# Kernel optimization log

Hardware: AMD Instinct MI355X
Metric: run time of the kernel (lower is better)

Reference implementation:

```python
import jax, jax.numpy as jnp
import numpy as np


def setup_inputs() -> dict:
    key = jax.random.key(0)
    ks = jax.random.split(key, 6)
    B, T, E = 4, 1024, 1024
    H, D = 16, 64  # num_heads = embed_size // head_size
    s = 0.02
    x = jax.random.normal(ks[0], (B, T, E), dtype=jnp.float32)
    Wq = jax.random.normal(ks[1], (H, D, E), dtype=jnp.float32) * s
    Wk = jax.random.normal(ks[2], (H, D, E), dtype=jnp.float32) * s
    Wv = jax.random.normal(ks[3], (H, D, E), dtype=jnp.float32) * s
    Wp = jax.random.normal(ks[4], (E, E), dtype=jnp.float32) * s
    bp = jnp.zeros((E,), dtype=jnp.float32)
    return {"x": x, "Wq": Wq, "Wk": Wk, "Wv": Wv, "Wp": Wp, "bp": bp}


def reference(x, Wq, Wk, Wv, Wp, bp):
    # x: [B, T, E]; Wq/Wk/Wv: [H, D, E] (per-head Linear(E, D, bias=False) weights)
    B, T, E = x.shape
    H, D, _ = Wq.shape
    scale = 1.0 / jnp.sqrt(jnp.asarray(D, dtype=x.dtype))
    # per-head projections, vectorized over heads (same math as the ModuleList loop)
    q = jnp.einsum('bte,hde->bhtd', x, Wq)
    k = jnp.einsum('bte,hde->bhtd', x, Wk)
    v = jnp.einsum('bte,hde->bhtd', x, Wv)
    scores = jnp.einsum('bhtd,bhsd->bhts', q, k) * scale  # [B,H,T,T]
    causal = jnp.tril(jnp.ones((T, T), dtype=bool))
    scores = jnp.where(causal[None, None], scores, jnp.finfo(x.dtype).min)
    att = jax.nn.softmax(scores, axis=-1)  # attention dropout: identity in eval
    o = jnp.einsum('bhts,bhsd->bhtd', att, v)
    # concat heads along channel dim (head order = module list order)
    o = o.transpose(0, 2, 1, 3).reshape(B, T, H * D)
    # output projection (nn.Linear: y = o @ Wp.T + bp); dropout: identity in eval
    return o @ Wp.T + bp
```

## Files before the change

kernel.cpp:

```cpp
#include <hip/hip_runtime.h>


#define T_SZ 1024
#define E_SZ 1024
#define H_SZ 16
#define D_SZ 64

typedef __attribute__((ext_vector_type(8))) short bf16x8;
typedef __attribute__((ext_vector_type(4))) short bf16x4;
typedef __attribute__((ext_vector_type(4))) float f32x4;

static __device__ __forceinline__ unsigned short f2b(float f) {
  unsigned int u = __builtin_bit_cast(unsigned int, f);
  u += 0x7fffu + ((u >> 16) & 1u);
  return (unsigned short)(u >> 16);
}

static __device__ __forceinline__ unsigned int cvt_pk(float lo, float hi) {
  unsigned int r;
  asm("v_cvt_pk_bf16_f32 %0, %1, %2" : "=v"(r) : "v"(lo), "v"(hi));
  return r;
}

static __device__ __forceinline__ void load_lds16(const void* g, void* l) {
  __builtin_amdgcn_global_load_lds(
      (const __attribute__((address_space(1))) void*)g,
      (__attribute__((address_space(3))) void*)l, 16, 0, 0);
}

__global__ void cast_all(const float* __restrict__ x, const float* __restrict__ wq,
                         const float* __restrict__ wk, const float* __restrict__ wv,
                         const float* __restrict__ wp,
                         unsigned short* __restrict__ xb,
                         unsigned short* __restrict__ wqkvb,
                         unsigned short* __restrict__ wpb) {
  int b = blockIdx.x;
  const float4* src;
  ushort4* dst;
  int i;
  if (b < 4096) {
    src = (const float4*)x; dst = (ushort4*)xb; i = b * 256 + threadIdx.x;
  } else {
    int a = (b - 4096) >> 10;
    i = ((b - 4096) & 1023) * 256 + threadIdx.x;
    src = (const float4*)(a == 0 ? wq : a == 1 ? wk : a == 2 ? wv : wp);
    dst = (ushort4*)(a == 3 ? wpb : wqkvb + (size_t)a * 1048576);
  }
  float4 v = src[i];
  ushort4 o;
  o.x = f2b(v.x); o.y = f2b(v.y); o.z = f2b(v.z); o.w = f2b(v.w);
  dst[i] = o;
}

template <int EPI, int BN>
__global__ void gemm_bt(const unsigned short* __restrict__ A,
                        const unsigned short* __restrict__ Bm,
                        int M, int N, int K,
                        float* __restrict__ outF, const float* __restrict__ bias,
                        unsigned short* __restrict__ Qb,
                        unsigned short* __restrict__ Kb,
                        unsigned short* __restrict__ Vtb) {
  constexpr int ASZ = 16384;
  constexpr int BSZ = BN * 128;
  constexpr int SLOT = ASZ + BSZ;
  constexpr int NN = BN / 32;
  __shared__ __align__(16) char lds[2 * SLOT];
  const int tid = threadIdx.x;
  const int wid = tid >> 6;
  const int lane = tid & 63;
  const int llo = lane & 15, lhi = lane >> 4;
  const int row0 = blockIdx.x * 128, col0 = blockIdx.y * BN;
  const int wr = (wid >> 1) * 64, wc = (wid & 1) * (BN / 2);
  const int swl = ((llo >> 2) & 3) << 5;

  f32x4 acc[4][NN];
#pragma unroll
  for (int m = 0; m < 4; ++m)
#pragma unroll
    for (int n = 0; n < NN; ++n) {
      f32x4 z = {0.f, 0.f, 0.f, 0.f};
      acc[m][n] = z;
    }

  auto stage = [&](int kt, char* base) {
#pragma unroll
    for (int c = 0; c < 4; ++c) {
      int off = c * 4096 + tid * 16;
      int r = off >> 7, cb = off & 127;
      int sb = cb ^ (((r >> 2) & 3) << 5);
      load_lds16((const char*)A + ((size_t)(row0 + r) * K + kt) * 2 + sb,
                 base + c * 4096 + wid * 1024);
    }
#pragma unroll
    for (int c = 0; c < BSZ / 4096; ++c) {
      int off = c * 4096 + tid * 16;
      int r = off >> 7, cb = off & 127;
      int sb = cb ^ (((r >> 2) & 3) << 5);
      load_lds16((const char*)Bm + ((size_t)(col0 + r) * K + kt) * 2 + sb,
                 base + ASZ + c * 4096 + wid * 1024);
    }
  };

  stage(0, lds);
  __syncthreads();
  int buf = 0;

  for (int kt = 0; kt < K; kt += 64) {
    char* cur = lds + buf * SLOT;
    if (kt + 64 < K) stage(kt + 64, lds + (buf ^ 1) * SLOT);

    bf16x8 af[4][2], bfr[NN][2];
#pragma unroll
    for (int m = 0; m < 4; ++m)
#pragma unroll
      for (int kk = 0; kk < 2; ++kk)
        af[m][kk] = *reinterpret_cast<const bf16x8*>(
            cur + (wr + m * 16 + llo) * 128 + ((kk * 64 + lhi * 16) ^ swl));
#pragma unroll
    for (int n = 0; n < NN; ++n)
#pragma unroll
      for (int kk = 0; kk < 2; ++kk)
        bfr[n][kk] = *reinterpret_cast<const bf16x8*>(
            cur + ASZ + (wc + n * 16 + llo) * 128 + ((kk * 64 + lhi * 16) ^ swl));
#pragma unroll
    for (int m = 0; m < 4; ++m)
#pragma unroll
      for (int n = 0; n < NN; ++n)
#pragma unroll
        for (int kk = 0; kk < 2; ++kk)
          acc[m][n] = __builtin_amdgcn_mfma_f32_16x16x32_bf16(af[m][kk], bfr[n][kk],
                                                              acc[m][n], 0, 0, 0);
    __syncthreads();
    buf ^= 1;
  }

#pragma unroll
  for (int m = 0; m < 4; ++m)
#pragma unroll
    for (int n = 0; n < NN; ++n) {
      const int grow0 = row0 + wr + m * 16 + lhi * 4;
      const int gcol = col0 + wc + n * 16 + llo;
      if (EPI == 0) {
        int b = grow0 >> 10, t0 = grow0 & 1023;
        int which = gcol >> 10, hd = gcol & 1023;
        int h = hd >> 6, d = hd & 63;
        if (which == 2) {
          unsigned int w0 = cvt_pk(acc[m][n][0], acc[m][n][1]);
          unsigned int w1 = cvt_pk(acc[m][n][2], acc[m][n][3]);
          unsigned long long pk = ((unsigned long long)w1 << 32) | w0;
          *reinterpret_cast<unsigned long long*>(
              Vtb + (((size_t)(b * H_SZ + h)) * D_SZ + d) * T_SZ + t0) = pk;
        } else {
          unsigned short* dst = which ? Kb : Qb;
#pragma unroll
          for (int r = 0; r < 4; ++r)
            dst[(((size_t)(b * H_SZ + h)) * T_SZ + t0 + r) * D_SZ + d] =
                f2b(acc[m][n][r]);
        }
      } else {
#pragma unroll
        for (int r = 0; r < 4; ++r)
          outF[(size_t)(grow0 + r) * N + gcol] = acc[m][n][r] + bias[gcol];
      }
    }
}

__global__ void attn_kernel(const unsigned short* __restrict__ Q,
                            const unsigned short* __restrict__ K,
                            const unsigned short* __restrict__ Vt,
                            unsigned short* __restrict__ O) {
  __shared__ __align__(16) char smem[32768];
  const int tid = threadIdx.x, wid = tid >> 6, lane = tid & 63;
  const int llo = lane & 15, lhi = lane >> 4;
  const int f = blockIdx.y * 8 + blockIdx.x;
  const int xcd = f & 7, s = f >> 3;
  const int bh = xcd * 8 + (s & 7);
  const int j = s >> 3;
  const int blkx = (j < 4) ? (7 - j) : (j - 4);
  const size_t bhbase = (size_t)bh * (T_SZ * D_SZ);
  char* Ks = smem;
  char* Vs = smem + 8192;
  char* Ps = smem + 16384 + wid * 2048;

  const int qrow = blkx * 128 + wid * 16 + llo;
  const int myqt = 2 * blkx + (wid >> 2);
  const int last = 2 * blkx + 1;
  bf16x8 bq[2];
  {
    const unsigned short* qp = Q + bhbase + (size_t)qrow * D_SZ + lhi * 8;
    bq[0] = *reinterpret_cast<const bf16x8*>(qp);
    bq[1] = *reinterpret_cast<const bf16x8*>(qp + 32);
  }

  const int soff = tid * 16;
  const int srow = soff >> 7;
  const int sinb = soff & 127;
  const int slds = srow * 128 + (sinb ^ ((srow & 7) << 4));

  bf16x8 kreg, vreg;
  kreg = *reinterpret_cast<const bf16x8*>(K + bhbase + (size_t)srow * D_SZ + (sinb >> 1));
  vreg = *reinterpret_cast<const bf16x8*>(Vt + bhbase + (size_t)srow * T_SZ + (sinb >> 1));

  f32x4 oacc[4];
#pragma unroll
  for (int dc = 0; dc < 4; ++dc) {
    f32x4 z = {0.f, 0.f, 0.f, 0.f};
    oacc[dc] = z;
  }
  float mrun = -1e30f, lrun = 0.f;
  const float scale = 0.125f;

  for (int it = 0; it <= last; ++it) {
    __syncthreads();
    *reinterpret_cast<bf16x8*>(Ks + slds) = kreg;
    *reinterpret_cast<bf16x8*>(Vs + slds) = vreg;
    if (it < last) {
      const int kv = (it + 1) * 64;
      kreg = *reinterpret_cast<const bf16x8*>(
          K + bhbase + (size_t)(kv + srow) * D_SZ + (sinb >> 1));
      vreg = *reinterpret_cast<const bf16x8*>(
          Vt + bhbase + (size_t)srow * T_SZ + kv + (sinb >> 1));
    }
    __syncthreads();

    const int kv = it * 64;
    if (it <= myqt) {
      f32x4 sacc[4];
#pragma unroll
      for (int c = 0; c < 4; ++c) { f32x4 z = {0.f, 0.f, 0.f, 0.f}; sacc[c] = z; }
      __builtin_amdgcn_s_setprio(1);
#pragma unroll
      for (int seg = 0; seg < 2; ++seg)
#pragma unroll
        for (int c = 0; c < 4; ++c) {
          int key = c * 16 + llo;
          bf16x8 ak = *reinterpret_cast<const bf16x8*>(
              Ks + key * 128 + ((seg * 64 + lhi * 16) ^ ((key & 7) << 4)));
          sacc[c] = __builtin_amdgcn_mfma_f32_16x16x32_bf16(ak, bq[seg], sacc[c], 0, 0, 0);
        }
      __builtin_amdgcn_s_setprio(0);

      const bool diag = (it == myqt);
      float p[4][4];
      float pm = -1e30f;
#pragma unroll
      for (int c = 0; c < 4; ++c)
#pragma unroll
        for (int r = 0; r < 4; ++r) {
          float s2 = sacc[c][r] * scale;
          if (diag && (kv + c * 16 + lhi * 4 + r > qrow)) s2 = -1e30f;
          p[c][r] = s2;
          pm = fmaxf(pm, s2);
        }
      pm = fmaxf(pm, __shfl_xor(pm, 16, 64));
      pm = fmaxf(pm, __shfl_xor(pm, 32, 64));
      if (!__all(pm - mrun <= 8.0f)) {
        float mnew = fmaxf(mrun, pm);
        float alpha = __expf(mrun - mnew);
        mrun = mnew;
        lrun *= alpha;
#pragma unroll
        for (int dc = 0; dc < 4; ++dc)
#pragma unroll
          for (int r = 0; r < 4; ++r) oacc[dc][r] *= alpha;
      }

      float ps = 0.f;
#pragma unroll
      for (int c = 0; c < 4; ++c) {
#pragma unroll
        for (int r = 0; r < 4; ++r) {
          p[c][r] = __expf(p[c][r] - mrun);
          ps += p[c][r];
        }
        unsigned int w0 = cvt_pk(p[c][0], p[c][1]);
        unsigned int w1 = cvt_pk(p[c][2], p[c][3]);
        unsigned long long packed = ((unsigned long long)w1 << 32) | w0;
        *reinterpret_cast<bf16x4*>(
            Ps + llo * 128 + ((c * 32 + lhi * 8) ^ ((llo & 7) << 4))) =
            __builtin_bit_cast(bf16x4, packed);
      }
      asm volatile("s_waitcnt lgkmcnt(0)" ::: "memory");
      __builtin_amdgcn_sched_barrier(0);

      ps += __shfl_xor(ps, 16, 64);
      ps += __shfl_xor(ps, 32, 64);
      lrun += ps;

      __builtin_amdgcn_s_setprio(1);
#pragma unroll
      for (int seg = 0; seg < 2; ++seg) {
        bf16x8 bp = *reinterpret_cast<const bf16x8*>(
            Ps + llo * 128 + ((seg * 64 + lhi * 16) ^ ((llo & 7) << 4)));
#pragma unroll
        for (int dc = 0; dc < 4; ++dc) {
          int d = dc * 16 + llo;
          bf16x8 av = *reinterpret_cast<const bf16x8*>(
              Vs + d * 128 + ((seg * 64 + lhi * 16) ^ ((d & 7) << 4)));
          oacc[dc] = __builtin_amdgcn_mfma_f32_16x16x32_bf16(av, bp, oacc[dc], 0, 0, 0);
        }
      }
      __builtin_amdgcn_s_setprio(0);
    }
  }

  const int b = bh >> 4, h = bh & 15;
  float inv = 1.f / lrun;
#pragma unroll
  for (int dc = 0; dc < 4; ++dc) {
    unsigned int w0 = cvt_pk(oacc[dc][0] * inv, oacc[dc][1] * inv);
    unsigned int w1 = cvt_pk(oacc[dc][2] * inv, oacc[dc][3] * inv);
    unsigned int* op = reinterpret_cast<unsigned int*>(
        O + ((size_t)b * T_SZ + qrow) * E_SZ + h * D_SZ + dc * 16 + lhi * 4);
    op[0] = w0;
    op[1] = w1;
  }
}

extern "C" void kernel_launch(void* const* d_in, const int* in_sizes, int n_in,
                              void* d_out, int out_size, void* d_ws, size_t ws_size,
                              hipStream_t stream) {
  const float* x  = (const float*)d_in[0];
  const float* Wq = (const float*)d_in[1];
  const float* Wk = (const float*)d_in[2];
  const float* Wv = (const float*)d_in[3];
  const float* Wp = (const float*)d_in[4];
  const float* bp = (const float*)d_in[5];
  float* out = (float*)d_out;

  char* ws = (char*)d_ws;
  unsigned short* xb   = (unsigned short*)(ws);
  unsigned short* wqkv = (unsigned short*)(ws + (8u << 20));
  unsigned short* wp   = (unsigned short*)(ws + (14u << 20));
  unsigned short* Qb   = (unsigned short*)(ws + (16u << 20));
  unsigned short* Kb   = (unsigned short*)(ws + (24u << 20));
  unsigned short* Vtb  = (unsigned short*)(ws + (32u << 20));
  unsigned short* Ob   = (unsigned short*)(ws + (40u << 20));

  cast_all<<<8192, 256, 0, stream>>>(x, Wq, Wk, Wv, Wp, xb, wqkv, wp);

  gemm_bt<0, 128><<<dim3(32, 24), 256, 0, stream>>>(xb, wqkv, 4096, 3072, 1024,
                                                    nullptr, nullptr, Qb, Kb, Vtb);
  attn_kernel<<<dim3(8, 64), 512, 0, stream>>>(Qb, Kb, Vtb, Ob);
  gemm_bt<1, 64><<<dim3(32, 16), 256, 0, stream>>>(Ob, wp, 4096, 1024, 1024,
                                                   out, bp, nullptr, nullptr, nullptr);
}
```

Measured before the change: 81.73 us.

## Add 256x256-tile 8-wave pipelined QKV GEMM with half-tile LDS staging

Replaces the 128x128 QKV projection GEMM with a dedicated 256x256-tile kernel of 512 threads, 128KB LDS and an 8-phase ping-pong schedule. Each phase loads fragments, issues the next half-K stage load, and runs its MFMAs at raised priority between barriers. The aim is higher arithmetic intensity per global byte and overlap of loads with matrix math. The cost is a grid of only 192 blocks on a 256-CU part, so some CUs sit idle, plus heavy register and LDS use per block.

```diff
diff --git a/kernel.cpp b/kernel.cpp
--- a/kernel.cpp
+++ b/kernel.cpp
@@ -52,14 +52,162 @@
   dst[i] = o;
 }
 
-template <int EPI, int BN>
+template <int S, int KK, int FH>
+static __device__ __forceinline__ void ph_load(const char* lds0, int wr, int wc,
+                                               int llo, int lhi, int swl,
+                                               bf16x8 (&af)[4], bf16x8 (&bfr)[4]) {
+  const char* ab = lds0 + S * 65536 + KK * 16384;
+  const char* bb = ab + 32768;
+#pragma unroll
+  for (int m = 0; m < 4; ++m)
+    af[m] = *reinterpret_cast<const bf16x8*>(
+        ab + (wr + (FH * 4 + m) * 16 + llo) * 64 + ((lhi * 16) ^ swl));
+#pragma unroll
+  for (int n = 0; n < 4; ++n)
+    bfr[n] = *reinterpret_cast<const bf16x8*>(
+        bb + (wc + n * 16 + llo) * 64 + ((lhi * 16) ^ swl));
+}
+template <int FH>
+static __device__ __forceinline__ void ph_mfma(const bf16x8 (&af)[4],
+                                               const bf16x8 (&bfr)[4],
+                                               f32x4 (&acc)[8][4]) {
+#pragma unroll
+  for (int m = 0; m < 4; ++m)
+#pragma unroll
+    for (int n = 0; n < 4; ++n)
+      acc[FH * 4 + m][n] = __builtin_amdgcn_mfma_f32_16x16x32_bf16(
+          af[m], bfr[n], acc[FH * 4 + m][n], 0, 0, 0);
+}
+
+__global__ __launch_bounds__(512) void gemm256_qkv(const unsigned short* __restrict__ A,
+                                                   const unsigned short* __restrict__ Bm,
+                                                   unsigned short* __restrict__ Qb,
+                                                   unsigned short* __restrict__ Kb,
+                                                   unsigned short* __restrict__ Vtb) {
+  constexpr int K = 1024;
+  __shared__ __align__(16) char lds[131072];
+  const int tid = threadIdx.x, wid = tid >> 6, lane = tid & 63;
+  const int llo = lane & 15, lhi = lane >> 4;
+  const int row0 = blockIdx.x * 256, col0 = blockIdx.y * 256;
+  const int wr = (wid >> 2) * 128, wc = (wid & 3) * 64;
+  const int swl = ((llo & 3) ^ ((llo >> 2) & 3)) << 4;
+
+  f32x4 acc[8][4];
+#pragma unroll
+  for (int m = 0; m < 8; ++m)
+#pragma unroll
+    for (int n = 0; n < 4; ++n) {
+      f32x4 z = {0.f, 0.f, 0.f, 0.f};
+      acc[m][n] = z;
+    }
+
+  auto stageh = [&](const unsigned short* src, int rb, int t, int h, int op) {
+    char* dst = lds + (t & 1) * 65536 + op * 32768 + h * 16384 + wid * 1024;
+    const int kt = t * 64 + h * 32;
+#pragma unroll
+    for (int c = 0; c < 2; ++c) {
+      int off = c * 8192 + tid * 16;
+      int r = off >> 6, cb = off & 63;
+      int sb = cb ^ ((((r & 3) ^ ((r >> 2) & 3)) << 4));
+      load_lds16((const char*)src + ((size_t)(rb + r) * K + kt) * 2 + sb,
+                 dst + c * 8192);
+    }
+  };
+
+  stageh(A, row0, 0, 0, 0); stageh(Bm, col0, 0, 0, 1);
+  stageh(A, row0, 0, 1, 0); stageh(Bm, col0, 0, 1, 1);
+  stageh(A, row0, 1, 0, 0); stageh(Bm, col0, 1, 0, 1);
+  asm volatile("s_waitcnt vmcnt(4)" ::: "memory");
+  __builtin_amdgcn_s_barrier();
+
+#pragma unroll 1
+  for (int j = 0; j < 8; ++j) {
+    const bool lj = (j == 7);
+    { bf16x8 af[4], bfr[4];
+      ph_load<0, 0, 0>(lds, wr, wc, llo, lhi, swl, af, bfr);
+      stageh(A, row0, 2 * j + 1, 1, 0);
+      __builtin_amdgcn_s_barrier();
+      __builtin_amdgcn_s_setprio(1); ph_mfma<0>(af, bfr, acc); __builtin_amdgcn_s_setprio(0);
+      __builtin_amdgcn_s_barrier(); }
+    { bf16x8 af[4], bfr[4];
+      ph_load<0, 0, 1>(lds, wr, wc, llo, lhi, swl, af, bfr);
+      stageh(Bm, col0, 2 * j + 1, 1, 1);
+      __builtin_amdgcn_s_barrier();
+      __builtin_amdgcn_s_setprio(1); ph_mfma<1>(af, bfr, acc); __builtin_amdgcn_s_setprio(0);
+      __builtin_amdgcn_s_barrier(); }
+    { bf16x8 af[4], bfr[4];
+      ph_load<0, 1, 0>(lds, wr, wc, llo, lhi, swl, af, bfr);
+      if (!lj) stageh(A, row0, 2 * j + 2, 0, 0);
+      __builtin_amdgcn_s_barrier();
+      __builtin_amdgcn_s_setprio(1); ph_mfma<0>(af, bfr, acc); __builtin_amdgcn_s_setprio(0);
+      __builtin_amdgcn_s_barrier(); }
+    { bf16x8 af[4], bfr[4];
+      ph_load<0, 1, 1>(lds, wr, wc, llo, lhi, swl, af, bfr);
+      if (!lj) stageh(Bm, col0, 2 * j + 2, 0, 1);
+      if (lj) asm volatile("s_waitcnt vmcnt(0)" ::: "memory");
+      else    asm volatile("s_waitcnt vmcnt(4)" ::: "memory");
+      __builtin_amdgcn_s_barrier();
+      __builtin_amdgcn_s_setprio(1); ph_mfma<1>(af, bfr, acc); __builtin_amdgcn_s_setprio(0);
+      __builtin_amdgcn_s_barrier(); }
+    { bf16x8 af[4], bfr[4];
+      ph_load<1, 0, 0>(lds, wr, wc, llo, lhi, swl, af, bfr);
+      if (!lj) stageh(A, row0, 2 * j + 2, 1, 0);
+      __builtin_amdgcn_s_barrier();
+      __builtin_amdgcn_s_setprio(1); ph_mfma<0>(af, bfr, acc); __builtin_amdgcn_s_setprio(0);
+      __builtin_amdgcn_s_barrier(); }
+    { bf16x8 af[4], bfr[4];
+      ph_load<1, 0, 1>(lds, wr, wc, llo, lhi, swl, af, bfr);
+      if (!lj) stageh(Bm, col0, 2 * j + 2, 1, 1);
+      __builtin_amdgcn_s_barrier();
+      __builtin_amdgcn_s_setprio(1); ph_mfma<1>(af, bfr, acc); __builtin_amdgcn_s_setprio(0);
+      __builtin_amdgcn_s_barrier(); }
+    { bf16x8 af[4], bfr[4];
+      ph_load<1, 1, 0>(lds, wr, wc, llo, lhi, swl, af, bfr);
+      if (!lj) stageh(A, row0, 2 * j + 3, 0, 0);
+      __builtin_amdgcn_s_barrier();
+      __builtin_amdgcn_s_setprio(1); ph_mfma<0>(af, bfr, acc); __builtin_amdgcn_s_setprio(0);
+      __builtin_amdgcn_s_barrier(); }
+    { bf16x8 af[4], bfr[4];
+      ph_load<1, 1, 1>(lds, wr, wc, llo, lhi, swl, af, bfr);
+      if (!lj) {
+        stageh(Bm, col0, 2 * j + 3, 0, 1);
+        asm volatile("s_waitcnt vmcnt(4)" ::: "memory");
+      }
+      __builtin_amdgcn_s_barrier();
+      __builtin_amdgcn_s_setprio(1); ph_mfma<1>(af, bfr, acc); __builtin_amdgcn_s_setprio(0);
+      __builtin_amdgcn_s_barrier(); }
+  }
+
+#pragma unroll
+  for (int mf = 0; mf < 8; ++mf)
+#pragma unroll
+    for (int nf = 0; nf < 4; ++nf) {
+      const int grow0 = row0 + wr + mf * 16 + lhi * 4;
+      const int gcol = col0 + wc + nf * 16 + llo;
+      int b = grow0 >> 10, t0 = grow0 & 1023;
+      int which = gcol >> 10, hd = gcol & 1023;
+      int h = hd >> 6, d = hd & 63;
+      if (which == 2) {
+        unsigned int w0 = cvt_pk(acc[mf][nf][0], acc[mf][nf][1]);
+        unsigned int w1 = cvt_pk(acc[mf][nf][2], acc[mf][nf][3]);
+        unsigned long long pk = ((unsigned long long)w1 << 32) | w0;
+        *reinterpret_cast<unsigned long long*>(
+            Vtb + (((size_t)(b * H_SZ + h)) * D_SZ + d) * T_SZ + t0) = pk;
+      } else {
+        unsigned short* dst = which ? Kb : Qb;
+#pragma unroll
+        for (int r = 0; r < 4; ++r)
+          dst[(((size_t)(b * H_SZ + h)) * T_SZ + t0 + r) * D_SZ + d] =
+              f2b(acc[mf][nf][r]);
+      }
+    }
+}
+
+template <int BN>
 __global__ void gemm_bt(const unsigned short* __restrict__ A,
                         const unsigned short* __restrict__ Bm,
                         int M, int N, int K,
-                        float* __restrict__ outF, const float* __restrict__ bias,
-                        unsigned short* __restrict__ Qb,
-                        unsigned short* __restrict__ Kb,
-                        unsigned short* __restrict__ Vtb) {
+                        float* __restrict__ outF, const float* __restrict__ bias) {
   constexpr int ASZ = 16384;
   constexpr int BSZ = BN * 128;
   constexpr int SLOT = ASZ + BSZ;
@@ -140,28 +288,9 @@
     for (int n = 0; n < NN; ++n) {
       const int grow0 = row0 + wr + m * 16 + lhi * 4;
       const int gcol = col0 + wc + n * 16 + llo;
-      if (EPI == 0) {
-        int b = grow0 >> 10, t0 = grow0 & 1023;
-        int which = gcol >> 10, hd = gcol & 1023;
-        int h = hd >> 6, d = hd & 63;
-        if (which == 2) {
-          unsigned int w0 = cvt_pk(acc[m][n][0], acc[m][n][1]);
-          unsigned int w1 = cvt_pk(acc[m][n][2], acc[m][n][3]);
-          unsigned long long pk = ((unsigned long long)w1 << 32) | w0;
-          *reinterpret_cast<unsigned long long*>(
-              Vtb + (((size_t)(b * H_SZ + h)) * D_SZ + d) * T_SZ + t0) = pk;
-        } else {
-          unsigned short* dst = which ? Kb : Qb;
-#pragma unroll
-          for (int r = 0; r < 4; ++r)
-            dst[(((size_t)(b * H_SZ + h)) * T_SZ + t0 + r) * D_SZ + d] =
-                f2b(acc[m][n][r]);
-        }
-      } else {
-#pragma unroll
-        for (int r = 0; r < 4; ++r)
-          outF[(size_t)(grow0 + r) * N + gcol] = acc[m][n][r] + bias[gcol];
-      }
+#pragma unroll
+      for (int r = 0; r < 4; ++r)
+        outF[(size_t)(grow0 + r) * N + gcol] = acc[m][n][r] + bias[gcol];
     }
 }
 
@@ -339,9 +468,7 @@
 
   cast_all<<<8192, 256, 0, stream>>>(x, Wq, Wk, Wv, Wp, xb, wqkv, wp);
 
-  gemm_bt<0, 128><<<dim3(32, 24), 256, 0, stream>>>(xb, wqkv, 4096, 3072, 1024,
-                                                    nullptr, nullptr, Qb, Kb, Vtb);
+  gemm256_qkv<<<dim3(16, 12), 512, 0, stream>>>(xb, wqkv, Qb, Kb, Vtb);
   attn_kernel<<<dim3(8, 64), 512, 0, stream>>>(Qb, Kb, Vtb, Ob);
-  gemm_bt<1, 64><<<dim3(32, 16), 256, 0, stream>>>(Ob, wp, 4096, 1024, 1024,
-                                                   out, bp, nullptr, nullptr, nullptr);
-}
+  gemm_bt<64><<<dim3(32, 16), 256, 0, stream>>>(Ob, wp, 4096, 1024, 1024, out, bp);
+}
```

After: 92.06 us. 1.13x slower.
